# Optimization experiments

Measured on AMD Instinct MI355X. Metric: run time of the kernel, lower is better.

## Reference

```python
import jax, jax.numpy as jnp
import numpy as np

B, T, F, H = 2048, 16, 768, 1024  # batch(nodes), timesteps, 3*input_size, hidden_size


def setup_inputs() -> dict:
    key = jax.random.key(0)
    k1, k2, k3 = jax.random.split(key, 3)
    s_ih = 1.0 / np.sqrt(F)
    s_hh = 1.0 / np.sqrt(H)
    return {
        "x": jax.random.normal(k1, (B, T, F), dtype=jnp.float32),
        "W_ih": jax.random.normal(k2, (F, 4 * H), dtype=jnp.float32) * s_ih,
        "W_hh": jax.random.normal(k3, (H, 4 * H), dtype=jnp.float32) * s_hh,
        "b": jnp.zeros((4 * H,), dtype=jnp.float32),
    }


def reference(x, W_ih, W_hh, b):
    # Batched equivalent of the original per-sample python loop:
    # each sample's [T, F] sequence runs through the LSTM; the final hidden
    # state [H] per sample is concatenated and reshaped to (-1, B).
    Bb, Tt, Ff = x.shape
    Hh = W_hh.shape[0]
    x_t = jnp.swapaxes(x, 0, 1)  # [T, B, F]

    def step(carry, xt):
        h, c = carry
        gates = xt @ W_ih + h @ W_hh + b  # [B, 4H]
        i, f, g, o = jnp.split(gates, 4, axis=-1)
        c = jax.nn.sigmoid(f) * c + jax.nn.sigmoid(i) * jnp.tanh(g)
        h = jax.nn.sigmoid(o) * jnp.tanh(c)
        return (h, c), None

    h0 = jnp.zeros((Bb, Hh), dtype=x.dtype)
    (h, _), _ = jax.lax.scan(step, (h0, h0), x_t)
    # torch.cat over batch of [H] vectors -> flat [B*H], then reshape(-1, B)
    return h.reshape(-1).reshape(-1, Bb)
```

## Files before the change

### kernel.cpp

```cpp
#include <hip/hip_runtime.h>
#include <hip/hip_bf16.h>
#include <stdint.h>

#define B_  2048
#define T_  16
#define F_  768
#define H_  1024
#define G4_ 4096

typedef __attribute__((ext_vector_type(8))) __bf16 bf16x8;
typedef __attribute__((ext_vector_type(4))) float  f32x4;

static __device__ __forceinline__ unsigned short f2bf(float f) {
    union { float f; uint32_t u; } v; v.f = f;
    uint32_t u = v.u;
    uint32_t r = (u + 0x7fffu + ((u >> 16) & 1u)) >> 16;
    return (unsigned short)r;
}
static __device__ __forceinline__ unsigned short f2h(float f) {
    union { _Float16 h; unsigned short u; } v; v.h = (_Float16)f; return v.u;
}
static __device__ __forceinline__ float h2f(unsigned short u) {
    union { _Float16 h; unsigned short u; } v; v.u = u; return (float)v.h;
}
static __device__ __forceinline__ float sigf(float x) {
    return 1.0f / (1.0f + __expf(-x));
}
static __device__ __forceinline__ float tanhfast(float x) {
    return 2.0f / (1.0f + __expf(-2.0f * x)) - 1.0f;
}

#define GLOAD_LDS16(gsrc, ldst)                                                       \
    __builtin_amdgcn_global_load_lds((const __attribute__((address_space(1))) void*)(gsrc), \
                                     (__attribute__((address_space(3))) void*)(ldst), \
                                     16, 0, 0)


__global__ void convert_x_kernel(const float* __restrict__ x,
                                 unsigned short* __restrict__ xbf, int n4) {
    int idx = blockIdx.x * blockDim.x + threadIdx.x;
    if (idx >= n4) return;
    float4 v = *(const float4*)(x + (size_t)idx * 4);
    ushort4 o;
    o.x = f2bf(v.x); o.y = f2bf(v.y); o.z = f2bf(v.z); o.w = f2bf(v.w);
    *(ushort4*)(xbf + (size_t)idx * 4) = o;
}

__global__ void transpose_w_kernel(const float* __restrict__ w,
                                   unsigned short* __restrict__ wt, int K, int mode) {
    __shared__ float tile[32][33];
    int nb = blockIdx.x * 32;
    int kb = blockIdx.y * 32;
    int tx = threadIdx.x, ty = threadIdx.y;
    #pragma unroll
    for (int i = 0; i < 32; i += 8)
        tile[ty + i][tx] = w[(size_t)(kb + ty + i) * G4_ + nb + tx];
    __syncthreads();
    #pragma unroll
    for (int i = 0; i < 32; i += 8) {
        int n = nb + ty + i;
        int g = n >> 10;
        int j = n & 1023;
        int np = mode ? ((j >> 4) * 64 + g * 16 + (j & 15))
                      : ((j >> 6) * 256 + g * 64 + ((j >> 4) & 3) * 16 + (j & 15));
        wt[(size_t)np * K + kb + tx] = f2bf(tile[tx][ty + i]);
    }
}


#define STAGE4(bufi, kind, half, gbase, ld, rowbase, kt) do {                         \
    const int kel_ = (kt) * 64;                                                       \
    _Pragma("unroll")                                                                 \
    for (int r2 = 0; r2 < 2; ++r2) {                                                  \
        const int rih_ = r2 * 64 + (tid >> 3);                                        \
        const int ch_  = (tid & 7) ^ (rih_ & 7);                                      \
        GLOAD_LDS16((gbase) + (size_t)((rowbase) + (half) * 128 + rih_) * (ld)        \
                            + kel_ + ch_ * 8,                                         \
                    &lds[bufi][kind][half][r2 * 4096 + tid * 8]);                     \
    }                                                                                 \
} while (0)

#define RD4_A(half_, mb)                                                              \
    _Pragma("unroll")                                                                 \
    for (int mm = 0; mm < 4; ++mm) {                                                  \
        const int row_ = ((mb) + mm) * 32 + wm * 16 + fr;                             \
        _Pragma("unroll")                                                             \
        for (int kk = 0; kk < 2; ++kk)                                                \
            Afr[mm][kk] = *(const bf16x8*)&lds[buf][0][half_]                         \
                [(row_ & 127) * 64 + (((kk * 4 + fq) ^ (row_ & 7)) * 8)];             \
    }

#define RD4_B(half_, nb)                                                              \
    _Pragma("unroll")                                                                 \
    for (int nn = 0; nn < 2; ++nn) {                                                  \
        const int row_ = ((nb) + nn) * 64 + wn * 16 + fr;                             \
        _Pragma("unroll")                                                             \
        for (int kk = 0; kk < 2; ++kk)                                                \
            Bfr[(nb) + nn][kk] = *(const bf16x8*)&lds[buf][1][half_]                  \
                [(row_ & 127) * 64 + (((kk * 4 + fq) ^ (row_ & 7)) * 8)];             \
    }

#define MFMAQ(mb, nb)                                                                 \
    __builtin_amdgcn_s_setprio(1);                                                    \
    _Pragma("unroll")                                                                 \
    for (int mm = 0; mm < 4; ++mm)                                                    \
        _Pragma("unroll")                                                             \
        for (int nn = 0; nn < 2; ++nn)                                                \
            _Pragma("unroll")                                                         \
            for (int kk = 0; kk < 2; ++kk)                                            \
                acc[(mb) + mm][(nb) + nn] = __builtin_amdgcn_mfma_f32_16x16x32_bf16(  \
                    Afr[mm][kk], Bfr[(nb) + nn][kk], acc[(mb) + mm][(nb) + nn], 0, 0, 0); \
    __builtin_amdgcn_s_setprio(0);

#define WAITV4  asm volatile("s_waitcnt vmcnt(10)" ::: "memory");                     \
                __builtin_amdgcn_sched_barrier(0);
#define BARR4   __builtin_amdgcn_s_barrier();                                         \
                __builtin_amdgcn_sched_barrier(0);

#define KLOOP4(ABASE, ALD, BBASE, BLD, NT)                                            \
    STAGE4(0, 0, 0, ABASE, ALD, bm0, 0);                                              \
    STAGE4(0, 1, 0, BBASE, BLD, bn0, 0);                                              \
    STAGE4(0, 1, 1, BBASE, BLD, bn0, 0);                                              \
    STAGE4(0, 0, 1, ABASE, ALD, bm0, 0);                                              \
    STAGE4(1, 0, 0, ABASE, ALD, bm0, 1);                                              \
    STAGE4(1, 1, 0, BBASE, BLD, bn0, 1);                                              \
    STAGE4(1, 1, 1, BBASE, BLD, bn0, 1);                                              \
    WAITV4; BARR4;                                                                    \
    for (int kt = 0; kt < (NT); ++kt) {                                               \
        const int buf = kt & 1, nbuf = buf ^ 1;                                       \
        const int k1 = (kt + 1 < (NT)) ? kt + 1 : (NT) - 1;                           \
        const int k2 = (kt + 2 < (NT)) ? kt + 2 : (NT) - 1;                           \
        bf16x8 Afr[4][2]; bf16x8 Bfr[4][2];                                           \
                                                                             \
        RD4_A(0, 0); RD4_B(0, 0);                                                     \
        STAGE4(nbuf, 0, 1, ABASE, ALD, bm0, k1);                                      \
        WAITV4; BARR4;                                                                \
        MFMAQ(0, 0); BARR4;                                                           \
                                                                             \
        RD4_B(1, 2);                                                                  \
        STAGE4(buf, 0, 0, ABASE, ALD, bm0, k2);                                       \
        WAITV4; BARR4;                                                                \
        MFMAQ(0, 2); BARR4;                                                           \
                                                                             \
        RD4_A(1, 4);                                                                  \
        STAGE4(buf, 1, 0, BBASE, BLD, bn0, k2);                                       \
        BARR4;                                                                        \
        MFMAQ(4, 0); BARR4;                                                           \
                                                                             \
        STAGE4(buf, 1, 1, BBASE, BLD, bn0, k2);                                       \
        WAITV4; BARR4;                                                                \
        MFMAQ(4, 2); BARR4;                                                           \
    }

__global__ __launch_bounds__(512, 2) void xgemm8_kernel(
        const unsigned short* __restrict__ xbf,
        const unsigned short* __restrict__ wih_t,
        unsigned short* __restrict__ gx) {
    __shared__ __align__(16) unsigned short lds[2][2][2][8192];

    const int bid = blockIdx.x;
    const int xcd = bid & 7;
    const int i   = bid >> 3;
    const int bmg = i >> 6;
    const int r   = i & 63;
    const int bn  = r >> 2;
    const int bm  = xcd * 16 + bmg * 4 + (r & 3);
    const int bm0 = bm * 256, bn0 = bn * 256;

    const int tid = threadIdx.x;
    const int wid = tid >> 6, lane = tid & 63;
    const int wm = wid >> 2, wn = wid & 3;
    const int fr = lane & 15, fq = lane >> 4;

    f32x4 acc[8][4] = {};

    KLOOP4(xbf, F_, wih_t, F_, 12)

    const int j = bn * 64 + wn * 16 + fr;
    #pragma unroll
    for (int mm = 0; mm < 8; ++mm) {
        #pragma unroll
        for (int rr = 0; rr < 4; ++rr) {
            int row = bm0 + mm * 32 + wm * 16 + fq * 4 + rr;
            int tt = row & 15, bb = row >> 4;
            ushort4 o;
            o.x = f2h(acc[mm][0][rr]);
            o.y = f2h(acc[mm][1][rr]);
            o.z = f2h(acc[mm][2][rr]);
            o.w = f2h(acc[mm][3][rr]);
            *(ushort4*)(gx + (((size_t)tt * B_ + bb) * H_ + j) * 4) = o;
        }
    }
}


#define STAGE_A6(slot, kt) do {                                                       \
    const int kel_ = (kt) * 64;                                                       \
    _Pragma("unroll")                                                                 \
    for (int r2 = 0; r2 < 2; ++r2) {                                                  \
        const int rih_ = r2 * 32 + (tid >> 3);                                        \
        const int ch_  = (tid & 7) ^ (rih_ & 7);                                      \
        GLOAD_LDS16(SRC_A + (size_t)(bm0 + rih_) * H_ + kel_ + ch_ * 8,               \
                    &ldsA[slot][r2 * 2048 + tid * 8]);                                \
    }                                                                                 \
} while (0)

#define STAGE_B6(slot, kt) do {                                                       \
    const int kel_ = (kt) * 64;                                                       \
    _Pragma("unroll")                                                                 \
    for (int r4 = 0; r4 < 4; ++r4) {                                                  \
        const int rih_ = r4 * 32 + (tid >> 3);                                        \
        const int ch_  = (tid & 7) ^ (rih_ & 7);                                      \
        GLOAD_LDS16(SRC_B + (size_t)(bn0 + rih_) * H_ + kel_ + ch_ * 8,               \
                    &ldsB[slot][r4 * 2048 + tid * 8]);                                \
    }                                                                                 \
} while (0)

#define RD_A6(slot, AR)                                                               \
    _Pragma("unroll")                                                                 \
    for (int mm = 0; mm < 2; ++mm) {                                                  \
        const int row_ = wm * 32 + mm * 16 + fr;                                      \
        _Pragma("unroll")                                                             \
        for (int kk = 0; kk < 2; ++kk)                                                \
            AR[mm][kk] = *(const bf16x8*)&ldsA[slot]                                  \
                [row_ * 64 + (((kk * 4 + fq) ^ (row_ & 7)) * 8)];                     \
    }

#define RD_B6(slot, BF)                                                               \
    _Pragma("unroll")                                                                 \
    for (int nf = 0; nf < 4; ++nf) {                                                  \
        const int rowb_ = wn * 64 + nf * 16 + fr;                                     \
        _Pragma("unroll")                                                             \
        for (int kk = 0; kk < 2; ++kk)                                                \
            BF[nf][kk] = *(const bf16x8*)&ldsB[slot]                                  \
                [rowb_ * 64 + (((kk * 4 + fq) ^ (rowb_ & 7)) * 8)];                   \
    }

#define MFMA16S(AR, BF)                                                               \
    __builtin_amdgcn_s_setprio(1);                                                    \
    _Pragma("unroll")                                                                 \
    for (int mm = 0; mm < 2; ++mm)                                                    \
        _Pragma("unroll")                                                             \
        for (int nf = 0; nf < 4; ++nf)                                                \
            _Pragma("unroll")                                                         \
            for (int kk = 0; kk < 2; ++kk)                                            \
                acc[mm][nf] = __builtin_amdgcn_mfma_f32_16x16x32_bf16(                \
                    AR[mm][kk], BF[nf][kk], acc[mm][nf], 0, 0, 0);                    \
    __builtin_amdgcn_s_setprio(0);

#define WAIT6 asm volatile("s_waitcnt vmcnt(6)" ::: "memory");
#define LGKM0 asm volatile("s_waitcnt lgkmcnt(0)" ::: "memory");
#define BARR  __builtin_amdgcn_s_barrier();

#define KTILE6(KT, NT) do {                                                           \
    const int s_  = (KT) % 3;                                                         \
    const int s2_ = ((KT) + 2) % 3;                                                   \
    const int k2_ = ((KT) + 2 < (NT)) ? (KT) + 2 : (NT) - 1;                          \
    bf16x8 Am[2][2], Bf[4][2];                                                        \
    RD_A6(s_, Am);                                                                    \
    RD_B6(s_, Bf);                                                                    \
    STAGE_A6(s2_, k2_);                                                               \
    STAGE_B6(s2_, k2_);                                                               \
    LGKM0;                                                                            \
    MFMA16S(Am, Bf);                                                                  \
    WAIT6; BARR;                                                                      \
} while (0)

__global__ __launch_bounds__(256, 2) void lstm_step6_kernel(
        const unsigned short* __restrict__ hprev,
        const unsigned short* __restrict__ whh_t,
        const unsigned short* __restrict__ gx,
        const float* __restrict__ bias,
        float* __restrict__ c,
        unsigned short* __restrict__ hnext,
        float* __restrict__ hout,
        int t, int last) {
    __shared__ __align__(16) unsigned short ldsA[3][4096];
    __shared__ __align__(16) unsigned short ldsB[3][8192];

    const int bid = blockIdx.x;
    const int xcd = bid & 7;
    const int i   = bid >> 3;
    const int bn  = xcd * 4 + (i & 3);
    const int bm  = i >> 2;
    const int bm0 = bm * 64, bn0 = bn * 128;

    const int tid = threadIdx.x;
    const int wid = tid >> 6, lane = tid & 63;
    const int wm = wid >> 1, wn = wid & 1;
    const int fr = lane & 15, fq = lane >> 4;

    const unsigned short* __restrict__ SRC_A = hprev;
    const unsigned short* __restrict__ SRC_B = whh_t;

    f32x4 acc[2][4] = {};

    STAGE_A6(0, 0); STAGE_B6(0, 0);
    STAGE_A6(1, 1); STAGE_B6(1, 1);
    WAIT6; BARR;

    for (int kt = 0; kt < 16; ++kt) KTILE6(kt, 16);

    const int j = (bn * 2 + wn) * 16 + fr;
    const float b_i = bias[j];
    const float b_f = bias[H_ + j];
    const float b_g = bias[2 * H_ + j];
    const float b_o = bias[3 * H_ + j];

    #pragma unroll
    for (int mm = 0; mm < 2; ++mm) {
        #pragma unroll
        for (int rr = 0; rr < 4; ++rr) {
            int row = bm0 + wm * 32 + mm * 16 + fq * 4 + rr;
            ushort4 g4 = *(const ushort4*)(gx + (((size_t)t * B_ + row) * H_ + j) * 4);
            float gi = acc[mm][0][rr] + b_i + h2f(g4.x);
            float gf = acc[mm][1][rr] + b_f + h2f(g4.y);
            float gg = acc[mm][2][rr] + b_g + h2f(g4.z);
            float go = acc[mm][3][rr] + b_o + h2f(g4.w);
            size_t off = (size_t)row * H_ + j;
            float cold = c[off];
            float cn = sigf(gf) * cold + sigf(gi) * tanhfast(gg);
            float hv = sigf(go) * tanhfast(cn);
            c[off] = cn;
            hnext[off] = f2bf(hv);
            if (last) hout[off] = hv;
        }
    }
}


__global__ void cell0_kernel(const unsigned short* __restrict__ gx,
                             const float* __restrict__ bias,
                             float* __restrict__ c,
                             unsigned short* __restrict__ hbf) {
    int idx = blockIdx.x * blockDim.x + threadIdx.x;
    int b = idx >> 10;
    int j = idx & 1023;
    ushort4 g4 = *(const ushort4*)(gx + ((size_t)b * H_ + j) * 4);
    float gi = bias[j]          + h2f(g4.x);
    float gg = bias[2 * H_ + j] + h2f(g4.z);
    float go = bias[3 * H_ + j] + h2f(g4.w);
    float cn = sigf(gi) * tanhfast(gg);
    float hv = sigf(go) * tanhfast(cn);
    size_t off = (size_t)b * H_ + j;
    c[off] = cn;
    hbf[off] = f2bf(hv);
}


extern "C" void kernel_launch(void* const* d_in, const int* in_sizes, int n_in,
                              void* d_out, int out_size, void* d_ws, size_t ws_size,
                              hipStream_t stream) {
    const float* x    = (const float*)d_in[0];
    const float* Wih  = (const float*)d_in[1];
    const float* Whh  = (const float*)d_in[2];
    const float* bias = (const float*)d_in[3];
    float* out = (float*)d_out;

    char* ws = (char*)d_ws;
    unsigned short* xbf   = (unsigned short*)(ws);
    unsigned short* wih_t = (unsigned short*)(ws + 50331648);
    unsigned short* whh_t = (unsigned short*)(ws + 56623104);
    unsigned short* hbf0  = (unsigned short*)(ws + 65011712);
    unsigned short* hbf1  = (unsigned short*)(ws + 69206016);
    float*          c     = (float*)(ws + 73400320);
    unsigned short* gx    = (unsigned short*)(ws + 81788928);

    int n4 = B_ * T_ * F_ / 4;
    hipLaunchKernelGGL(convert_x_kernel, dim3((n4 + 255) / 256), dim3(256), 0, stream,
                       x, xbf, n4);
    hipLaunchKernelGGL(transpose_w_kernel, dim3(G4_ / 32, F_ / 32), dim3(32, 8), 0, stream,
                       Wih, wih_t, F_, 0);
    hipLaunchKernelGGL(transpose_w_kernel, dim3(G4_ / 32, H_ / 32), dim3(32, 8), 0, stream,
                       Whh, whh_t, H_, 1);

    hipLaunchKernelGGL(xgemm8_kernel, dim3(2048), dim3(512), 0, stream,
                       xbf, wih_t, gx);

    hipLaunchKernelGGL(cell0_kernel, dim3(B_ * H_ / 256), dim3(256), 0, stream,
                       gx, bias, c, hbf0);

    for (int t = 1; t < T_; ++t) {
        unsigned short* hr = (t & 1) ? hbf0 : hbf1;
        unsigned short* hw = (t & 1) ? hbf1 : hbf0;
        hipLaunchKernelGGL(lstm_step6_kernel, dim3(1024), dim3(256), 0, stream,
                           hr, whh_t, gx, bias, c, hw, out, t, (t == T_ - 1) ? 1 : 0);
    }
}
```

Measured before the change: 780.3 us.

## Make GEMM blocks compute two N tiles each, pipelining across tile boundary

Both the input-projection GEMM and the per-step recurrent GEMM now have each block process two consecutive output column tiles in one continuous software-pipelined K loop. Grid sizes are halved accordingly. The first tile's epilogue runs mid-loop while loads for the second tile are already in flight, and the gx/c loads for the cell update are issued early so their latency is hidden behind MFMAs. This removes one pipeline prologue/drain per tile and lowers block launch and tail overhead. In exchange it uses more registers for the prefetched values, halves the number of blocks available to fill the CUs, and relies on hand-tuned vmcnt counts that must match the number of loads in flight.

```diff
diff --git a/kernel.cpp b/kernel.cpp
--- a/kernel.cpp
+++ b/kernel.cpp
@@ -117,42 +117,26 @@
 #define BARR4   __builtin_amdgcn_s_barrier();                                         \
                 __builtin_amdgcn_sched_barrier(0);
 
-#define KLOOP4(ABASE, ALD, BBASE, BLD, NT)                                            \
-    STAGE4(0, 0, 0, ABASE, ALD, bm0, 0);                                              \
-    STAGE4(0, 1, 0, BBASE, BLD, bn0, 0);                                              \
-    STAGE4(0, 1, 1, BBASE, BLD, bn0, 0);                                              \
-    STAGE4(0, 0, 1, ABASE, ALD, bm0, 0);                                              \
-    STAGE4(1, 0, 0, ABASE, ALD, bm0, 1);                                              \
-    STAGE4(1, 1, 0, BBASE, BLD, bn0, 1);                                              \
-    STAGE4(1, 1, 1, BBASE, BLD, bn0, 1);                                              \
-    WAITV4; BARR4;                                                                    \
-    for (int kt = 0; kt < (NT); ++kt) {                                               \
-        const int buf = kt & 1, nbuf = buf ^ 1;                                       \
-        const int k1 = (kt + 1 < (NT)) ? kt + 1 : (NT) - 1;                           \
-        const int k2 = (kt + 2 < (NT)) ? kt + 2 : (NT) - 1;                           \
-        bf16x8 Afr[4][2]; bf16x8 Bfr[4][2];                                           \
-                                                                             \
-        RD4_A(0, 0); RD4_B(0, 0);                                                     \
-        STAGE4(nbuf, 0, 1, ABASE, ALD, bm0, k1);                                      \
-        WAITV4; BARR4;                                                                \
-        MFMAQ(0, 0); BARR4;                                                           \
-                                                                             \
-        RD4_B(1, 2);                                                                  \
-        STAGE4(buf, 0, 0, ABASE, ALD, bm0, k2);                                       \
-        WAITV4; BARR4;                                                                \
-        MFMAQ(0, 2); BARR4;                                                           \
-                                                                             \
-        RD4_A(1, 4);                                                                  \
-        STAGE4(buf, 1, 0, BBASE, BLD, bn0, k2);                                       \
-        BARR4;                                                                        \
-        MFMAQ(4, 0); BARR4;                                                           \
-                                                                             \
-        STAGE4(buf, 1, 1, BBASE, BLD, bn0, k2);                                       \
-        WAITV4; BARR4;                                                                \
-        MFMAQ(4, 2); BARR4;                                                           \
-    }
-
-__global__ __launch_bounds__(512, 2) void xgemm8_kernel(
+#define EPIX(pbn)                                                                     \
+    {                                                                                 \
+        const int j_ = (pbn) * 64 + wn * 16 + fr;                                     \
+        _Pragma("unroll")                                                             \
+        for (int mm = 0; mm < 8; ++mm) {                                              \
+            _Pragma("unroll")                                                         \
+            for (int rr = 0; rr < 4; ++rr) {                                          \
+                int row_ = bm0 + mm * 32 + wm * 16 + fq * 4 + rr;                     \
+                int tt_ = row_ & 15, bb_ = row_ >> 4;                                 \
+                ushort4 o_;                                                           \
+                o_.x = f2h(acc[mm][0][rr]);                                           \
+                o_.y = f2h(acc[mm][1][rr]);                                           \
+                o_.z = f2h(acc[mm][2][rr]);                                           \
+                o_.w = f2h(acc[mm][3][rr]);                                           \
+                *(ushort4*)(gx + (((size_t)tt_ * B_ + bb_) * H_ + j_) * 4) = o_;      \
+            }                                                                         \
+        }                                                                             \
+    }
+
+__global__ __launch_bounds__(512, 2) void xgemm8p_kernel(
         const unsigned short* __restrict__ xbf,
         const unsigned short* __restrict__ wih_t,
         unsigned short* __restrict__ gx) {
@@ -161,11 +145,10 @@
     const int bid = blockIdx.x;
     const int xcd = bid & 7;
     const int i   = bid >> 3;
-    const int bmg = i >> 6;
-    const int r   = i & 63;
-    const int bn  = r >> 2;
-    const int bm  = xcd * 16 + bmg * 4 + (r & 3);
-    const int bm0 = bm * 256, bn0 = bn * 256;
+    const int bnp = i & 7;
+    const int bm  = xcd * 16 + (i >> 3);
+    const int bm0 = bm * 256;
+    const int bn00 = bnp * 512;
 
     const int tid = threadIdx.x;
     const int wid = tid >> 6, lane = tid & 63;
@@ -174,44 +157,70 @@
 
     f32x4 acc[8][4] = {};
 
-    KLOOP4(xbf, F_, wih_t, F_, 12)
-
-    const int j = bn * 64 + wn * 16 + fr;
-    #pragma unroll
-    for (int mm = 0; mm < 8; ++mm) {
-        #pragma unroll
-        for (int rr = 0; rr < 4; ++rr) {
-            int row = bm0 + mm * 32 + wm * 16 + fq * 4 + rr;
-            int tt = row & 15, bb = row >> 4;
-            ushort4 o;
-            o.x = f2h(acc[mm][0][rr]);
-            o.y = f2h(acc[mm][1][rr]);
-            o.z = f2h(acc[mm][2][rr]);
-            o.w = f2h(acc[mm][3][rr]);
-            *(ushort4*)(gx + (((size_t)tt * B_ + bb) * H_ + j) * 4) = o;
+    STAGE4(0, 0, 0, xbf, F_, bm0, 0);
+    STAGE4(0, 1, 0, wih_t, F_, bn00, 0);
+    STAGE4(0, 1, 1, wih_t, F_, bn00, 0);
+    STAGE4(0, 0, 1, xbf, F_, bm0, 0);
+    STAGE4(1, 0, 0, xbf, F_, bm0, 1);
+    STAGE4(1, 1, 0, wih_t, F_, bn00, 1);
+    STAGE4(1, 1, 1, wih_t, F_, bn00, 1);
+    WAITV4; BARR4;
+
+    for (int kt = 0; kt < 24; ++kt) {
+        const int buf = kt & 1, nbuf = buf ^ 1;
+        const int k1 = (kt + 1 < 24) ? kt + 1 : 23;
+        const int k2 = (kt + 2 < 24) ? kt + 2 : 23;
+        const int a1 = (k1 >= 12) ? k1 - 12 : k1;
+        const int a2 = (k2 >= 12) ? k2 - 12 : k2;
+        const int bb2 = bn00 + ((k2 >= 12) ? 256 : 0);
+        bf16x8 Afr[4][2]; bf16x8 Bfr[4][2];
+        RD4_A(0, 0); RD4_B(0, 0);
+        STAGE4(nbuf, 0, 1, xbf, F_, bm0, a1);
+        WAITV4; BARR4;
+        MFMAQ(0, 0); BARR4;
+        RD4_B(1, 2);
+        STAGE4(buf, 0, 0, xbf, F_, bm0, a2);
+        WAITV4; BARR4;
+        MFMAQ(0, 2); BARR4;
+        RD4_A(1, 4);
+        STAGE4(buf, 1, 0, wih_t, F_, bb2, a2);
+        BARR4;
+        MFMAQ(4, 0); BARR4;
+        STAGE4(buf, 1, 1, wih_t, F_, bb2, a2);
+        WAITV4; BARR4;
+        MFMAQ(4, 2); BARR4;
+        if (kt == 11) {
+            EPIX(bnp * 2);
+            #pragma unroll
+            for (int mm = 0; mm < 8; ++mm)
+                #pragma unroll
+                for (int nf = 0; nf < 4; ++nf)
+                    #pragma unroll
+                    for (int q = 0; q < 4; ++q) acc[mm][nf][q] = 0.0f;
         }
     }
-}
-
-
-#define STAGE_A6(slot, kt) do {                                                       \
+    EPIX(bnp * 2 + 1);
+}
+
+
+#define STA6(slot, kt) do {                                                           \
     const int kel_ = (kt) * 64;                                                       \
     _Pragma("unroll")                                                                 \
     for (int r2 = 0; r2 < 2; ++r2) {                                                  \
         const int rih_ = r2 * 32 + (tid >> 3);                                        \
         const int ch_  = (tid & 7) ^ (rih_ & 7);                                      \
-        GLOAD_LDS16(SRC_A + (size_t)(bm0 + rih_) * H_ + kel_ + ch_ * 8,               \
+        GLOAD_LDS16(hprev + (size_t)(bm0 + rih_) * H_ + kel_ + ch_ * 8,               \
                     &ldsA[slot][r2 * 2048 + tid * 8]);                                \
     }                                                                                 \
 } while (0)
 
-#define STAGE_B6(slot, kt) do {                                                       \
+#define STB6(slot, rowbase, kt) do {                                                  \
     const int kel_ = (kt) * 64;                                                       \
     _Pragma("unroll")                                                                 \
     for (int r4 = 0; r4 < 4; ++r4) {                                                  \
         const int rih_ = r4 * 32 + (tid >> 3);                                        \
         const int ch_  = (tid & 7) ^ (rih_ & 7);                                      \
-        GLOAD_LDS16(SRC_B + (size_t)(bn0 + rih_) * H_ + kel_ + ch_ * 8,               \
+        GLOAD_LDS16(whh_t + (size_t)((rowbase) + rih_) * H_ + kel_ + ch_ * 8,         \
                     &ldsB[slot][r4 * 2048 + tid * 8]);                                \
     }                                                                                 \
 } while (0)
@@ -248,25 +257,10 @@
                     AR[mm][kk], BF[nf][kk], acc[mm][nf], 0, 0, 0);                    \
     __builtin_amdgcn_s_setprio(0);
 
-#define WAIT6 asm volatile("s_waitcnt vmcnt(6)" ::: "memory");
 #define LGKM0 asm volatile("s_waitcnt lgkmcnt(0)" ::: "memory");
 #define BARR  __builtin_amdgcn_s_barrier();
 
-#define KTILE6(KT, NT) do {                                                           \
-    const int s_  = (KT) % 3;                                                         \
-    const int s2_ = ((KT) + 2) % 3;                                                   \
-    const int k2_ = ((KT) + 2 < (NT)) ? (KT) + 2 : (NT) - 1;                          \
-    bf16x8 Am[2][2], Bf[4][2];                                                        \
-    RD_A6(s_, Am);                                                                    \
-    RD_B6(s_, Bf);                                                                    \
-    STAGE_A6(s2_, k2_);                                                               \
-    STAGE_B6(s2_, k2_);                                                               \
-    LGKM0;                                                                            \
-    MFMA16S(Am, Bf);                                                                  \
-    WAIT6; BARR;                                                                      \
-} while (0)
-
-__global__ __launch_bounds__(256, 2) void lstm_step6_kernel(
+__global__ __launch_bounds__(256, 2) void lstm_step_dp_kernel(
         const unsigned short* __restrict__ hprev,
         const unsigned short* __restrict__ whh_t,
         const unsigned short* __restrict__ gx,
@@ -281,46 +275,101 @@
     const int bid = blockIdx.x;
     const int xcd = bid & 7;
     const int i   = bid >> 3;
-    const int bn  = xcd * 4 + (i & 3);
-    const int bm  = i >> 2;
-    const int bm0 = bm * 64, bn0 = bn * 128;
+    const int pair = i & 1;
+    const int bm  = i >> 1;
+    const int bn_base = xcd * 4 + pair * 2;
+    const int bm0 = bm * 64;
 
     const int tid = threadIdx.x;
     const int wid = tid >> 6, lane = tid & 63;
     const int wm = wid >> 1, wn = wid & 1;
     const int fr = lane & 15, fq = lane >> 4;
 
-    const unsigned short* __restrict__ SRC_A = hprev;
-    const unsigned short* __restrict__ SRC_B = whh_t;
+    const int j0 = (bn_base * 2 + wn) * 16 + fr;
+    const int j1 = ((bn_base + 1) * 2 + wn) * 16 + fr;
+    const float bi0 = bias[j0], bf0 = bias[H_ + j0], bg0 = bias[2 * H_ + j0], bo0 = bias[3 * H_ + j0];
+    const float bi1 = bias[j1], bf1 = bias[H_ + j1], bg1 = bias[2 * H_ + j1], bo1 = bias[3 * H_ + j1];
 
     f32x4 acc[2][4] = {};
-
-    STAGE_A6(0, 0); STAGE_B6(0, 0);
-    STAGE_A6(1, 1); STAGE_B6(1, 1);
-    WAIT6; BARR;
-
-    for (int kt = 0; kt < 16; ++kt) KTILE6(kt, 16);
-
-    const int j = (bn * 2 + wn) * 16 + fr;
-    const float b_i = bias[j];
-    const float b_f = bias[H_ + j];
-    const float b_g = bias[2 * H_ + j];
-    const float b_o = bias[3 * H_ + j];
+    ushort4 gpre[2][4];
+    float   cpre[2][4];
+
+    STA6(0, 0); STB6(0, bn_base * 128, 0);
+    STA6(1, 1); STB6(1, bn_base * 128, 1);
+    asm volatile("s_waitcnt vmcnt(6)" ::: "memory");
+    BARR;
+
+    for (int kt = 0; kt < 32; ++kt) {
+        const int s_  = kt % 3;
+        const int s2_ = (kt + 2) % 3;
+        const int k2  = (kt + 2 < 32) ? kt + 2 : 31;
+        const int ak2 = k2 & 15;
+        const int brb2 = (bn_base + (k2 >> 4)) * 128;
+        bf16x8 Am[2][2], Bf[4][2];
+        RD_A6(s_, Am);
+        RD_B6(s_, Bf);
+        STA6(s2_, ak2);
+        STB6(s2_, brb2, ak2);
+        if (kt == 13 || kt == 29) {
+            const int p_ = kt >> 4;
+            const int jp_ = p_ ? j1 : j0;
+            #pragma unroll
+            for (int mm = 0; mm < 2; ++mm)
+                #pragma unroll
+                for (int rr = 0; rr < 4; ++rr) {
+                    int row_ = bm0 + wm * 32 + mm * 16 + fq * 4 + rr;
+                    gpre[mm][rr] = *(const ushort4*)(gx + (((size_t)t * B_ + row_) * H_ + jp_) * 4);
+                    cpre[mm][rr] = c[(size_t)row_ * H_ + jp_];
+                }
+        }
+        LGKM0;
+        MFMA16S(Am, Bf);
+        if (kt == 13 || kt == 14 || kt == 29 || kt == 30)
+            asm volatile("s_waitcnt vmcnt(22)" ::: "memory");
+        else
+            asm volatile("s_waitcnt vmcnt(6)" ::: "memory");
+        BARR;
+        if (kt == 15) {
+            #pragma unroll
+            for (int mm = 0; mm < 2; ++mm) {
+                #pragma unroll
+                for (int rr = 0; rr < 4; ++rr) {
+                    int row_ = bm0 + wm * 32 + mm * 16 + fq * 4 + rr;
+                    ushort4 g4 = gpre[mm][rr];
+                    float gi = acc[mm][0][rr] + bi0 + h2f(g4.x);
+                    float gf = acc[mm][1][rr] + bf0 + h2f(g4.y);
+                    float gg = acc[mm][2][rr] + bg0 + h2f(g4.z);
+                    float go = acc[mm][3][rr] + bo0 + h2f(g4.w);
+                    float cn = sigf(gf) * cpre[mm][rr] + sigf(gi) * tanhfast(gg);
+                    float hv = sigf(go) * tanhfast(cn);
+                    size_t off = (size_t)row_ * H_ + j0;
+                    c[off] = cn;
+                    hnext[off] = f2bf(hv);
+                    if (last) hout[off] = hv;
+                }
+            }
+            #pragma unroll
+            for (int mm = 0; mm < 2; ++mm)
+                #pragma unroll
+                for (int nf = 0; nf < 4; ++nf)
+                    #pragma unroll
+                    for (int q = 0; q < 4; ++q) acc[mm][nf][q] = 0.0f;
+        }
+    }
 
     #pragma unroll
     for (int mm = 0; mm < 2; ++mm) {
         #pragma unroll
         for (int rr = 0; rr < 4; ++rr) {
-            int row = bm0 + wm * 32 + mm * 16 + fq * 4 + rr;
-            ushort4 g4 = *(const ushort4*)(gx + (((size_t)t * B_ + row) * H_ + j) * 4);
-            float gi = acc[mm][0][rr] + b_i + h2f(g4.x);
-            float gf = acc[mm][1][rr] + b_f + h2f(g4.y);
-            float gg = acc[mm][2][rr] + b_g + h2f(g4.z);
-            float go = acc[mm][3][rr] + b_o + h2f(g4.w);
-            size_t off = (size_t)row * H_ + j;
-            float cold = c[off];
-            float cn = sigf(gf) * cold + sigf(gi) * tanhfast(gg);
+            int row_ = bm0 + wm * 32 + mm * 16 + fq * 4 + rr;
+            ushort4 g4 = gpre[mm][rr];
+            float gi = acc[mm][0][rr] + bi1 + h2f(g4.x);
+            float gf = acc[mm][1][rr] + bf1 + h2f(g4.y);
+            float gg = acc[mm][2][rr] + bg1 + h2f(g4.z);
+            float go = acc[mm][3][rr] + bo1 + h2f(g4.w);
+            float cn = sigf(gf) * cpre[mm][rr] + sigf(gi) * tanhfast(gg);
             float hv = sigf(go) * tanhfast(cn);
+            size_t off = (size_t)row_ * H_ + j1;
             c[off] = cn;
             hnext[off] = f2bf(hv);
             if (last) hout[off] = hv;
@@ -374,7 +423,7 @@
     hipLaunchKernelGGL(transpose_w_kernel, dim3(G4_ / 32, H_ / 32), dim3(32, 8), 0, stream,
                        Whh, whh_t, H_, 1);
 
-    hipLaunchKernelGGL(xgemm8_kernel, dim3(2048), dim3(512), 0, stream,
+    hipLaunchKernelGGL(xgemm8p_kernel, dim3(1024), dim3(512), 0, stream,
                        xbf, wih_t, gx);
 
     hipLaunchKernelGGL(cell0_kernel, dim3(B_ * H_ / 256), dim3(256), 0, stream,
@@ -383,7 +432,7 @@
     for (int t = 1; t < T_; ++t) {
         unsigned short* hr = (t & 1) ? hbf0 : hbf1;
         unsigned short* hw = (t & 1) ? hbf1 : hbf0;
-        hipLaunchKernelGGL(lstm_step6_kernel, dim3(1024), dim3(256), 0, stream,
+        hipLaunchKernelGGL(lstm_step_dp_kernel, dim3(512), dim3(256), 0, stream,
                            hr, whh_t, gx, bias, c, hw, out, t, (t == T_ - 1) ? 1 : 0);
     }
 }
```

Result: slower. 841.1 us (+7.8%).
